# Performance work log

Hardware: AMD Instinct MI355X
Metric: run time of the kernel (lower is better)

The kernel has to match this reference:

```python
import jax, jax.numpy as jnp
import numpy as np

MARGIN = 0.3
WARMUP_EPOCHS = 10
K = 5
ALPHA = 2.0
SAME_CAM_NEG_BOOST = 1.2
NEG_INF = jnp.float32(-jnp.inf)
POS_INF = jnp.float32(jnp.inf)


def setup_inputs() -> dict:
    key = jax.random.key(0)
    k1, k2, k3 = jax.random.split(key, 3)
    N, D = 8192, 2048
    feats = jax.random.normal(k1, (N, D), dtype=jnp.float32)
    labels = jax.random.randint(k2, (N,), 0, 256, dtype=jnp.int64)
    camids = jax.random.randint(k3, (N,), 0, 8, dtype=jnp.int64)
    return {"feats": feats, "labels": labels, "camids": camids, "epoch": 20}


def _topk_mean(dist_mat, mask, k, largest):
    # dist_mat [N,N], mask [N,N] bool. Per-row mean of k largest/smallest valid elems.
    if largest:
        work = jnp.where(mask, dist_mat, NEG_INF)
        vals, _ = jax.lax.top_k(work, k)            # [N,k] largest
        fallback = jnp.max(work, axis=1)
    else:
        work = jnp.where(mask, dist_mat, POS_INF)
        vals = -jax.lax.top_k(-work, k)[0]          # [N,k] smallest
        fallback = jnp.min(work, axis=1)
    is_valid = jnp.isfinite(vals)
    safe_sum = jnp.sum(jnp.where(is_valid, vals, 0.0), axis=1)
    counts = jnp.maximum(is_valid.sum(axis=1), 1)
    mean = safe_sum / counts
    return jnp.where(is_valid.any(axis=1), mean, fallback)


def _forward(feats, labels, camids, epoch):
    # (1) L2 normalize
    norm = jnp.linalg.norm(feats, axis=-1, keepdims=True)
    x = feats / jnp.maximum(norm, 1e-12)
    # Euclidean distance matrix [N,N]
    sq = jnp.sum(x * x, axis=1)
    dist2 = sq[:, None] + sq[None, :] - 2.0 * (x @ x.T)
    dist = jnp.sqrt(jnp.maximum(dist2, 1e-12))
    # masks (constants w.r.t. grad)
    N = feats.shape[0]
    eye = jnp.eye(N, dtype=bool)
    same_label = labels[:, None] == labels[None, :]
    same_cam = camids[:, None] == camids[None, :]
    is_pos = same_label & ~eye & ~same_cam   # cross_cam_pos=True
    is_neg = ~same_label & ~eye
    # boosted same-camera negatives
    neg_bias = jnp.where(is_neg & same_cam, SAME_CAM_NEG_BOOST, 1.0)
    dist_neg_sel = dist / jnp.maximum(neg_bias, 1e-6)
    # (2) top-k hard mining
    d_ap = _topk_mean(dist, is_pos, K, largest=True)
    d_an = _topk_mean(dist_neg_sel, is_neg, K, largest=False)
    # (5) hardness-aware weighting (no grad)
    w = jax.lax.stop_gradient(jax.nn.sigmoid(ALPHA * (d_ap - d_an)))
    w = w / jnp.maximum(w.mean(), 1e-12)
    # (3) margin schedule
    if epoch is not None and epoch < WARMUP_EPOCHS:
        per_sample = jax.nn.softplus(-(d_an - d_ap))
    else:
        per_sample = jax.nn.relu(d_ap - d_an + MARGIN)  # MarginRankingLoss, y=1
    loss = jnp.mean(w * per_sample)
    return loss, jax.lax.stop_gradient(d_ap), jax.lax.stop_gradient(d_an)


def reference(feats, labels, camids, epoch):
    return _forward(feats, labels, camids, epoch)
```

## Files before the change

### kernel.cpp

```cpp
#include <hip/hip_runtime.h>
#include <hip/hip_bf16.h>
#include <stdint.h>

typedef float   floatx4  __attribute__((ext_vector_type(4)));
typedef float   floatx16 __attribute__((ext_vector_type(16)));
typedef int     intx4    __attribute__((ext_vector_type(4)));
typedef int     intx8    __attribute__((ext_vector_type(8)));
typedef _Float16 halfx8  __attribute__((ext_vector_type(8)));
typedef _Float16 halfx4  __attribute__((ext_vector_type(4)));
typedef _Float16 half2v  __attribute__((ext_vector_type(2)));

#define NROW 8192
#define NDIM 2048
#define BM 128
#define SLICE 64
#define NSLICE 32
#define NSTRIP 64
#define NTILE (NSTRIP*(NSTRIP+1)/2)
#define NPOSB 256
#define DT_LD 136
#define KL_SYM 64
#define SLOT_P 8
#define MERGE_BLOCKS 256
#define BOOST_INV 0.6944444444f

__device__ __forceinline__ void ins_desc(float (&a)[5], float v) {
#pragma unroll
    for (int k = 0; k < 5; ++k) { float hi = fmaxf(a[k], v); float lo = fminf(a[k], v); a[k] = hi; v = lo; }
}
__device__ __forceinline__ void ins_asc(float (&a)[5], float v) {
#pragma unroll
    for (int k = 0; k < 5; ++k) { float lo = fminf(a[k], v); float hi = fmaxf(a[k], v); a[k] = lo; v = hi; }
}

__device__ __forceinline__ int   h2bits(half2v v) { return __builtin_bit_cast(int, v); }
__device__ __forceinline__ half2v bits2h(int v)   { return __builtin_bit_cast(half2v, v); }
__device__ __forceinline__ void ins_desc2(half2v (&a)[5], half2v v) {
#pragma unroll
    for (int k = 0; k < 5; ++k) {
        half2v hi = __builtin_elementwise_max(a[k], v);
        half2v lo = __builtin_elementwise_min(a[k], v);
        a[k] = hi; v = lo;
    }
}
__device__ __forceinline__ void ins_asc2(half2v (&a)[5], half2v v) {
#pragma unroll
    for (int k = 0; k < 5; ++k) {
        half2v lo = __builtin_elementwise_min(a[k], v);
        half2v hi = __builtin_elementwise_max(a[k], v);
        a[k] = lo; v = hi;
    }
}

__device__ __forceinline__ void load_lds16(const void* g, void* l) {
    __builtin_amdgcn_global_load_lds((__attribute__((address_space(1))) void*)(void*)g,
                                     (__attribute__((address_space(3))) void*)l,
                                     16, 0, 0);
}

__global__ __launch_bounds__(256) void k_normalize(const float* __restrict__ feats,
                                                   unsigned char* __restrict__ xb,
                                                   float* __restrict__ sq) {
    const int lane = threadIdx.x & 63;
    const int row = (blockIdx.x << 2) + (threadIdx.x >> 6);
    const float* f = feats + (size_t)row * NDIM;
    float4 v[8];
    float ss = 0.f;
#pragma unroll
    for (int i = 0; i < 8; ++i) {
        v[i] = *(const float4*)(f + ((i << 6) + lane) * 4);
        ss += v[i].x * v[i].x + v[i].y * v[i].y + v[i].z * v[i].z + v[i].w * v[i].w;
    }
#pragma unroll
    for (int o = 32; o > 0; o >>= 1) ss += __shfl_xor(ss, o);
    float inv = 1.0f / fmaxf(sqrtf(ss), 1e-12f);
    if (lane == 0) sq[row] = ss * inv * inv;
    unsigned char* xo = xb + (size_t)row * NDIM;
#pragma unroll
    for (int i = 0; i < 8; ++i) {
        int w0 = __builtin_amdgcn_cvt_pk_fp8_f32(v[i].x * inv, v[i].y * inv, 0, false);
        w0     = __builtin_amdgcn_cvt_pk_fp8_f32(v[i].z * inv, v[i].w * inv, w0, true);
        *(int*)(xo + ((i << 6) + lane) * 4) = w0;
    }
}

__device__ __forceinline__ void scan_half_row_neg(const _Float16* Dt_,
        int srow, int shalf, float (&neg5)[5]) {
    const int s2 = 2 * (srow & 7);
    const int PINF2 = 0x7C007C00;
    half2v n5[5];
#pragma unroll
    for (int k = 0; k < 5; ++k) n5[k] = bits2h(PINF2);
#pragma unroll
    for (int c8 = 0; c8 < 8; ++c8) {
        const int pc = ((shalf * 8 + c8) + s2) & 15;
        intx4 v = *(const intx4*)(Dt_ + srow * DT_LD + pc * 8);
#pragma unroll
        for (int e = 0; e < 4; ++e) ins_asc2(n5, bits2h(v[e]));
    }
    half2v tn[5];
#pragma unroll
    for (int k = 0; k < 5; ++k)
        tn[k] = bits2h((int)__builtin_amdgcn_alignbit((unsigned)h2bits(n5[k]), (unsigned)h2bits(n5[k]), 16));
#pragma unroll
    for (int k = 0; k < 5; ++k) ins_asc2(n5, tn[k]);
#pragma unroll
    for (int k = 0; k < 5; ++k) neg5[k] = (float)n5[k][0];
}

__device__ __forceinline__ void emit_neg(float (&neg5)[5], int shalf,
        _Float16* negp, int gi, int slot) {
    float tn[5];
#pragma unroll
    for (int k = 0; k < 5; ++k) tn[k] = __shfl_xor(neg5[k], 1);
#pragma unroll
    for (int k = 0; k < 5; ++k) { if (tn[k] < neg5[4]) ins_asc(neg5, tn[k]); }
    if (shalf == 0) {
        const float PINF = __builtin_inff();
        halfx8 hn;
#pragma unroll
        for (int k = 0; k < 5; ++k) hn[k] = (_Float16)neg5[k];
        hn[5] = hn[6] = hn[7] = (_Float16)PINF;
        *(halfx8*)(negp + ((size_t)slot * NROW + gi) * SLOT_P) = hn;
    }
}

__global__ __launch_bounds__(256, 3) void k_main(
        const unsigned char* __restrict__ xb, const float* __restrict__ sq,
        const int* __restrict__ labels, const int* __restrict__ camids,
        _Float16* __restrict__ negp, _Float16* __restrict__ posf) {
    __shared__ __align__(16) char smem[51200];

    const int tid = threadIdx.x;
    const int w = tid >> 6, lane = tid & 63;
    const int m32 = lane & 31;
    const int hi = lane >> 5;
    const int key = (lane >> 1) & 3;
    const int p0 = ((2 * hi + key) & 3) * 16;
    const int p1 = ((2 * hi + 1 + key) & 3) * 16;
    const float FINF = __builtin_inff();
    const float NINF = -FINF;

    if (blockIdx.x < NPOSB) {
        char* stg0 = smem;
        _Float16* D2 = (_Float16*)(smem + 12288);
        int* mem = (int*)(smem + 21504);
        unsigned short* mlc = (unsigned short*)(smem + 21760);
        float* msq = (float*)(smem + 21888);
        int* cntp = (int*)(smem + 22144);

        const int L = blockIdx.x;
        if (tid == 0) *cntp = 0;
        __syncthreads();
        for (int i = tid; i < NROW; i += 256) {
            if (labels[i] == L) {
                int slot = atomicAdd(cntp, 1);
                if (slot < 64) mem[slot] = i;
            }
        }
        __syncthreads();
        const int cnt = min(*cntp, 64);
        if (tid < 64) {
            if (tid < cnt) {
                int gi = mem[tid];
                mlc[tid] = (unsigned short)((labels[gi] << 4) | camids[gi]);
                msq[tid] = sq[gi];
            } else {
                mem[tid] = 0; mlc[tid] = 0xFFFF; msq[tid] = 0.f;
            }
        }
        __syncthreads();

        const int wm = w >> 1, wn = w & 1;
        const int lr = lane >> 2;
        const int lcb = (((lane & 3) - ((lane >> 3) & 3)) & 3) * 16;
        const int myrow = mem[w * 16 + lr];

        auto pstage = [&](int buf, int koff) {
            load_lds16(xb + (size_t)myrow * NDIM + koff + lcb,
                       stg0 + (buf << 12) + w * 1024);
        };

        floatx16 acc;
#pragma unroll
        for (int r = 0; r < 16; ++r) acc[r] = 0.f;

        pstage(0, 0);
        pstage(1, SLICE);
        for (int s = 0; s < NSLICE; ++s) {
            if (s + 2 < NSLICE) {
                int bs = s + 2; bs -= (bs >= 3 ? 3 : 0); bs -= (bs >= 3 ? 3 : 0);
                pstage((s + 2) % 3, (s + 2) * SLICE);
            }
            if (s < NSLICE - 2)       asm volatile("s_waitcnt vmcnt(2)" ::: "memory");
            else if (s == NSLICE - 2) asm volatile("s_waitcnt vmcnt(1)" ::: "memory");
            else                      asm volatile("s_waitcnt vmcnt(0)" ::: "memory");
            __builtin_amdgcn_s_barrier();
            asm volatile("" ::: "memory");
            const char* Ab = stg0 + ((s % 3) << 12);
            const char* ap = Ab + (wm * 32 + m32) * SLICE;
            intx4 alo = *(const intx4*)(ap + p0);
            intx4 ahi = *(const intx4*)(ap + p1);
            intx8 af = __builtin_shufflevector(alo, ahi, 0, 1, 2, 3, 4, 5, 6, 7);
            const char* bp = Ab + (wn * 32 + m32) * SLICE;
            intx4 blo = *(const intx4*)(bp + p0);
            intx4 bhi = *(const intx4*)(bp + p1);
            intx8 bf = __builtin_shufflevector(blo, bhi, 0, 1, 2, 3, 4, 5, 6, 7);
            acc = __builtin_amdgcn_mfma_scale_f32_32x32x64_f8f6f4(af, bf, acc, 0, 0, 0, 127, 0, 127);
            asm volatile("" ::: "memory");
            __builtin_amdgcn_s_barrier();
            asm volatile("" ::: "memory");
        }

        {
            const int jl = (w & 1) * 32 + m32;
            const int lcj = (int)mlc[jl];
            const float sj = msq[jl];
            const int wm2 = w >> 1;
#pragma unroll
            for (int r = 0; r < 16; ++r) {
                const int il = wm2 * 32 + (r & 3) + 8 * (r >> 2) + 4 * hi;
                float d2 = fmaxf(msq[il] + sj - 2.0f * acc[r], 1e-12f);
                const int x = (int)mlc[il] ^ lcj;
                bool posv = ((x & 0xFFF0) == 0) & ((x & 15) != 0);
                D2[il * 72 + jl] = posv ? (_Float16)d2 : (_Float16)NINF;
            }
        }
        __syncthreads();

        {
            const int prow = tid >> 2, q = tid & 3;
            const int NINF2 = 0xFC00FC00;
            half2v p5h[5];
#pragma unroll
            for (int k = 0; k < 5; ++k) p5h[k] = bits2h(NINF2);
            const _Float16* dp = D2 + prow * 72 + q * 16;
            intx4 v0 = *(const intx4*)dp;
            intx4 v1 = *(const intx4*)(dp + 8);
#pragma unroll
            for (int e = 0; e < 4; ++e) ins_desc2(p5h, bits2h(v0[e]));
#pragma unroll
            for (int e = 0; e < 4; ++e) ins_desc2(p5h, bits2h(v1[e]));
            half2v tp[5];
#pragma unroll
            for (int k = 0; k < 5; ++k)
                tp[k] = bits2h((int)__builtin_amdgcn_alignbit((unsigned)h2bits(p5h[k]), (unsigned)h2bits(p5h[k]), 16));
#pragma unroll
            for (int k = 0; k < 5; ++k) ins_desc2(p5h, tp[k]);
            float p5[5];
#pragma unroll
            for (int k = 0; k < 5; ++k) p5[k] = (float)p5h[k][0];
#pragma unroll
            for (int o = 1; o <= 2; o <<= 1) {
                float tq[5];
#pragma unroll
                for (int k = 0; k < 5; ++k) tq[k] = __shfl_xor(p5[k], o);
#pragma unroll
                for (int k = 0; k < 5; ++k) { if (tq[k] > p5[4]) ins_desc(p5, tq[k]); }
            }
            if (q == 0 && prow < cnt) {
                halfx8 hp;
#pragma unroll
                for (int k = 0; k < 5; ++k) hp[k] = (_Float16)p5[k];
                hp[5] = hp[6] = hp[7] = (_Float16)NINF;
                *(halfx8*)(posf + (size_t)mem[prow] * SLOT_P) = hp;
            }
        }
        return;
    }

    _Float16* Dt = (_Float16*)smem;
    float* sqr_s = (float*)(smem + 49152);
    float* sqc_s = sqr_s + BM;
    unsigned short* labcam_a = (unsigned short*)(sqc_s + BM);
    unsigned short* labcam_b = labcam_a + BM;

    const int wm = w >> 1, wn = w & 1;

    int a, b;
    {
        int bx = blockIdx.x - NPOSB;
        int o = (bx & 7) * (NTILE / 8) + (bx >> 3);
        if (o < 1792) {
            int st = o >> 6;
            int SA = (int)((1.0f + sqrtf(8.0f * (float)st + 1.0f)) * 0.5f);
            while (SA * (SA - 1) / 2 > st) --SA;
            while (SA * (SA + 1) / 2 <= st) ++SA;
            int SB = st - SA * (SA - 1) / 2;
            int inner = o & 63;
            a = SA * 8 + (inner >> 3);
            b = SB * 8 + (inner & 7);
        } else {
            int idx = o - 1792;
            int st = idx / 36;
            int inner = idx - st * 36;
            int ia = (int)((sqrtf(8.0f * (float)inner + 1.0f) - 1.0f) * 0.5f);
            while (ia * (ia + 1) / 2 > inner) --ia;
            while ((ia + 1) * (ia + 2) / 2 <= inner) ++ia;
            int ib = inner - ia * (ia + 1) / 2;
            a = st * 8 + ia;
            b = st * 8 + ib;
        }
    }
    const int r0 = a * BM, c0 = b * BM;

    const int lr = lane >> 2;
    const int lc = (((lane & 3) - ((lane >> 3) & 3)) & 3) * 16;

    auto stage = [&](int buf, int koff) {
        char* Asb = smem + (buf << 14);
        char* Bsb = Asb + 8192;
#pragma unroll
        for (int q = 0; q < 2; ++q) {
            const int ra = w * 32 + q * 16;
            load_lds16(xb + (size_t)(r0 + ra + lr) * NDIM + koff + lc, Asb + ra * SLICE);
            load_lds16(xb + (size_t)(c0 + ra + lr) * NDIM + koff + lc, Bsb + ra * SLICE);
        }
    };

    if (tid < BM) {
        int gi = r0 + tid;
        sqr_s[tid] = sq[gi];
        labcam_a[tid] = (unsigned short)((labels[gi] << 4) | camids[gi]);
    } else {
        int t2 = tid - BM;
        int gj = c0 + t2;
        sqc_s[t2] = sq[gj];
        labcam_b[t2] = (unsigned short)((labels[gj] << 4) | camids[gj]);
    }

    stage(0, 0);
    stage(1, SLICE);

    const int srow = tid >> 1;
    const int shalf = tid & 1;

    floatx16 acc[2][2];
#pragma unroll
    for (int ti = 0; ti < 2; ++ti)
#pragma unroll
        for (int tj = 0; tj < 2; ++tj)
#pragma unroll
            for (int r = 0; r < 16; ++r) acc[ti][tj][r] = 0.f;

    int bc = 0;
    for (int s = 0; s < NSLICE; ++s) {
        if (s + 2 < NSLICE) {
            int bs = bc + 2; if (bs >= 3) bs -= 3;
            stage(bs, (s + 2) * SLICE);
        }
        if (s < NSLICE - 2)       asm volatile("s_waitcnt vmcnt(8)" ::: "memory");
        else if (s == NSLICE - 2) asm volatile("s_waitcnt vmcnt(4)" ::: "memory");
        else                      asm volatile("s_waitcnt vmcnt(0)" ::: "memory");
        __builtin_amdgcn_s_barrier();
        asm volatile("" ::: "memory");

        const char* Ab = smem + (bc << 14);
        const char* Bb = Ab + 8192;
        intx8 bf[2];
#pragma unroll
        for (int tj = 0; tj < 2; ++tj) {
            const char* bp = Bb + (wn * 64 + tj * 32 + m32) * SLICE;
            intx4 lo = *(const intx4*)(bp + p0);
            intx4 hi4 = *(const intx4*)(bp + p1);
            bf[tj] = __builtin_shufflevector(lo, hi4, 0, 1, 2, 3, 4, 5, 6, 7);
        }
        __builtin_amdgcn_s_setprio(1);
#pragma unroll
        for (int ti = 0; ti < 2; ++ti) {
            const char* ap = Ab + (wm * 64 + ti * 32 + m32) * SLICE;
            intx4 lo = *(const intx4*)(ap + p0);
            intx4 hi4 = *(const intx4*)(ap + p1);
            intx8 af = __builtin_shufflevector(lo, hi4, 0, 1, 2, 3, 4, 5, 6, 7);
            acc[ti][0] = __builtin_amdgcn_mfma_scale_f32_32x32x64_f8f6f4(
                af, bf[0], acc[ti][0], 0, 0, 0, 127, 0, 127);
            acc[ti][1] = __builtin_amdgcn_mfma_scale_f32_32x32x64_f8f6f4(
                af, bf[1], acc[ti][1], 0, 0, 0, 127, 0, 127);
        }
        __builtin_amdgcn_s_setprio(0);
        asm volatile("" ::: "memory");
        __builtin_amdgcn_s_barrier();
        asm volatile("" ::: "memory");
        bc = (bc + 1 == 3) ? 0 : bc + 1;
    }

    {
        const int jl0 = wn * 64 + m32, jl1 = jl0 + 32;
        const float sj0 = sqc_s[jl0], sj1 = sqc_s[jl1];
        const int lb0 = (int)labcam_b[jl0], lb1 = (int)labcam_b[jl1];
        const int jc0 = jl0 >> 3, j7_0 = jl0 & 7;
        const int jc1 = jl1 >> 3, j7_1 = jl1 & 7;
#pragma unroll
        for (int ti = 0; ti < 2; ++ti) {
#pragma unroll
            for (int r = 0; r < 16; ++r) {
                const int il = wm * 64 + ti * 32 + (r & 3) + 8 * (r >> 2) + 4 * hi;
                const float si = sqr_s[il];
                const int la = (int)labcam_a[il];
                const int rot = 2 * (il & 7);
                _Float16* drow = Dt + il * DT_LD;

                float d2 = fmaxf(si + sj0 - 2.0f * acc[ti][0][r], 1e-12f);
                int x = la ^ lb0;
                float nv = (x & 15) ? d2 : d2 * BOOST_INV;
                nv = (x & 0xFFF0) ? nv : FINF;
                acc[ti][0][r] = nv;
                drow[(((jc0 + rot) & 15) << 3) + j7_0] = (_Float16)nv;

                d2 = fmaxf(si + sj1 - 2.0f * acc[ti][1][r], 1e-12f);
                x = la ^ lb1;
                nv = (x & 15) ? d2 : d2 * BOOST_INV;
                nv = (x & 0xFFF0) ? nv : FINF;
                acc[ti][1][r] = nv;
                drow[(((jc1 + rot) & 15) << 3) + j7_1] = (_Float16)nv;
            }
        }
    }
    __syncthreads();

    float neg5[5];
    scan_half_row_neg(Dt, srow, shalf, neg5);
    emit_neg(neg5, shalf, negp, r0 + srow, b);

    if (a != b) {
        __syncthreads();
#pragma unroll
        for (int tj = 0; tj < 2; ++tj) {
#pragma unroll
            for (int ti = 0; ti < 2; ++ti) {
                const int jl = wn * 64 + tj * 32 + m32;
                const int cw2 = 2 * (jl & 7);
#pragma unroll
                for (int rq = 0; rq < 4; ++rq) {
                    const int base_row = wm * 64 + ti * 32 + 8 * rq + 4 * hi;
                    halfx4 h;
#pragma unroll
                    for (int e = 0; e < 4; ++e) h[e] = (_Float16)acc[ti][tj][rq * 4 + e];
                    const int pch = (((base_row >> 3) + cw2) & 15);
                    *(halfx4*)(Dt + jl * DT_LD + (pch << 3) + 4 * hi) = h;
                }
            }
        }
        __syncthreads();
        scan_half_row_neg(Dt, srow, shalf, neg5);
        emit_neg(neg5, shalf, negp, c0 + srow, a);
    }
}

__global__ __launch_bounds__(256) void k_merge_sym(const _Float16* __restrict__ negp,
        const _Float16* __restrict__ posf, const int* __restrict__ epoch_p,
        float* __restrict__ out, float* __restrict__ wsum_p, float* __restrict__ wpsum_p) {
    const int t = threadIdx.x;
    const int rl = t & 31;
    const int sg = t >> 5;
    const int row = blockIdx.x * 32 + rl;
    const float NINF = -__builtin_inff(), PINF = __builtin_inff();
    float n5[5] = {PINF, PINF, PINF, PINF, PINF};
    const size_t rbase = (size_t)row * SLOT_P;
#pragma unroll
    for (int s = 0; s < 8; ++s) {
        const size_t off = (size_t)(sg * 8 + s) * ((size_t)NROW * SLOT_P) + rbase;
        halfx8 nv = *(const halfx8*)(negp + off);
#pragma unroll
        for (int e = 0; e < 8; ++e) { float f = (float)nv[e]; if (f < n5[4]) ins_asc(n5, f); }
    }
    __shared__ __align__(16) _Float16 ln[32][8][8];
    const int sw = (sg + rl) & 7;
    {
        halfx8 hn;
#pragma unroll
        for (int k = 0; k < 5; ++k) hn[k] = (_Float16)n5[k];
        hn[5] = hn[6] = hn[7] = (_Float16)PINF;
        *(halfx8*)&ln[rl][sw][0] = hn;
    }
    __syncthreads();
    if (t < 32) {
        float N5[5] = {PINF, PINF, PINF, PINF, PINF};
#pragma unroll
        for (int g = 0; g < 8; ++g) {
            halfx8 nv = *(const halfx8*)&ln[t][g][0];
#pragma unroll
            for (int e = 0; e < 8; ++e) { float f = (float)nv[e]; if (f < N5[4]) ins_asc(N5, f); }
        }
        const int orow = blockIdx.x * 32 + t;
        halfx8 pv = *(const halfx8*)(posf + (size_t)orow * SLOT_P);
        float s = 0.f; int c = 0;
#pragma unroll
        for (int k = 0; k < 5; ++k) { float f = (float)pv[k]; bool fin = (f > NINF); s += fin ? sqrtf(f) : 0.f; c += fin ? 1 : 0; }
        float d_ap = (c > 0) ? s / (float)c : NINF;
        s = 0.f; c = 0;
#pragma unroll
        for (int k = 0; k < 5; ++k) { bool fin = (N5[k] < PINF); s += fin ? sqrtf(N5[k]) : 0.f; c += fin ? 1 : 0; }
        float d_an = (c > 0) ? s / (float)c : PINF;

        out[1 + orow] = d_ap;
        out[1 + NROW + orow] = d_an;
        float diff = d_ap - d_an;
        float w0 = 1.0f / (1.0f + expf(-2.0f * diff));
        float p;
        if (*epoch_p < 10) {
            p = fmaxf(diff, 0.0f) + log1pf(expf(-fabsf(diff)));
        } else {
            p = fmaxf(diff + 0.3f, 0.0f);
        }
        float wp = w0 * p;
#pragma unroll
        for (int o = 16; o > 0; o >>= 1) { w0 += __shfl_down(w0, o, 32); wp += __shfl_down(wp, o, 32); }
        if (t == 0) { wsum_p[blockIdx.x] = w0; wpsum_p[blockIdx.x] = wp; }
    }
}

__global__ void k_finalize(const float* __restrict__ wsum_p, const float* __restrict__ wpsum_p,
                           float* __restrict__ out) {
    const int t = threadIdx.x;
    float sw  = wsum_p[t] + wsum_p[t + 64] + wsum_p[t + 128] + wsum_p[t + 192];
    float swp = wpsum_p[t] + wpsum_p[t + 64] + wpsum_p[t + 128] + wpsum_p[t + 192];
#pragma unroll
    for (int o = 32; o > 0; o >>= 1) { sw += __shfl_down(sw, o); swp += __shfl_down(swp, o); }
    if (t == 0) {
        float M = fmaxf(sw / (float)NROW, 1e-12f);
        out[0] = swp / ((float)NROW * M);
    }
}

extern "C" void kernel_launch(void* const* d_in, const int* in_sizes, int n_in,
                              void* d_out, int out_size, void* d_ws, size_t ws_size,
                              hipStream_t stream) {
    const float* feats  = (const float*)d_in[0];
    const int*   labels = (const int*)d_in[1];
    const int*   camids = (const int*)d_in[2];
    const int*   epoch  = (const int*)d_in[3];
    float* out = (float*)d_out;
    char* ws = (char*)d_ws;

    unsigned char* xb = (unsigned char*)ws;
    float* sq = (float*)(ws + 16777216);
    const size_t NEG_HALVES = (size_t)KL_SYM * NROW * SLOT_P;
    _Float16* negp = (_Float16*)(ws + 16777216 + 32768);
    _Float16* posf = negp + NEG_HALVES;
    float* wsum_p  = (float*)((char*)(posf + (size_t)NROW * SLOT_P));
    float* wpsum_p = wsum_p + MERGE_BLOCKS;

    k_normalize<<<NROW / 4, 256, 0, stream>>>(feats, xb, sq);
    k_main<<<NPOSB + NTILE, 256, 0, stream>>>(xb, sq, labels, camids, negp, posf);
    k_merge_sym<<<MERGE_BLOCKS, 256, 0, stream>>>(negp, posf, epoch, out, wsum_p, wpsum_p);
    k_finalize<<<1, 64, 0, stream>>>(wsum_p, wpsum_p, out);
}
```

Baseline: 207.5 us.

## Load A operand directly into registers, stage only B through LDS

```diff
diff --git a/kernel.cpp b/kernel.cpp
--- a/kernel.cpp
+++ b/kernel.cpp
@@ -129,7 +129,7 @@
         const unsigned char* __restrict__ xb, const float* __restrict__ sq,
         const int* __restrict__ labels, const int* __restrict__ camids,
         _Float16* __restrict__ negp, _Float16* __restrict__ posf) {
-    __shared__ __align__(16) char smem[51200];
+    __shared__ __align__(16) char smem[36864];
 
     const int tid = threadIdx.x;
     const int w = tid >> 6, lane = tid & 63;
@@ -188,10 +188,7 @@
         pstage(0, 0);
         pstage(1, SLICE);
         for (int s = 0; s < NSLICE; ++s) {
-            if (s + 2 < NSLICE) {
-                int bs = s + 2; bs -= (bs >= 3 ? 3 : 0); bs -= (bs >= 3 ? 3 : 0);
-                pstage((s + 2) % 3, (s + 2) * SLICE);
-            }
+            if (s + 2 < NSLICE) pstage((s + 2) % 3, (s + 2) * SLICE);
             if (s < NSLICE - 2)       asm volatile("s_waitcnt vmcnt(2)" ::: "memory");
             else if (s == NSLICE - 2) asm volatile("s_waitcnt vmcnt(1)" ::: "memory");
             else                      asm volatile("s_waitcnt vmcnt(0)" ::: "memory");
@@ -270,7 +267,7 @@
     }
 
     _Float16* Dt = (_Float16*)smem;
-    float* sqr_s = (float*)(smem + 49152);
+    float* sqr_s = (float*)(smem + 34816);
     float* sqc_s = sqr_s + BM;
     unsigned short* labcam_a = (unsigned short*)(sqc_s + BM);
     unsigned short* labcam_b = labcam_a + BM;
@@ -304,20 +301,6 @@
     }
     const int r0 = a * BM, c0 = b * BM;
 
-    const int lr = lane >> 2;
-    const int lc = (((lane & 3) - ((lane >> 3) & 3)) & 3) * 16;
-
-    auto stage = [&](int buf, int koff) {
-        char* Asb = smem + (buf << 14);
-        char* Bsb = Asb + 8192;
-#pragma unroll
-        for (int q = 0; q < 2; ++q) {
-            const int ra = w * 32 + q * 16;
-            load_lds16(xb + (size_t)(r0 + ra + lr) * NDIM + koff + lc, Asb + ra * SLICE);
-            load_lds16(xb + (size_t)(c0 + ra + lr) * NDIM + koff + lc, Bsb + ra * SLICE);
-        }
-    };
-
     if (tid < BM) {
         int gi = r0 + tid;
         sqr_s[tid] = sq[gi];
@@ -329,8 +312,29 @@
         labcam_b[t2] = (unsigned short)((labels[gj] << 4) | camids[gj]);
     }
 
-    stage(0, 0);
-    stage(1, SLICE);
+    const int lr = lane >> 2;
+    const int lc = (((lane & 3) - ((lane >> 3) & 3)) & 3) * 16;
+    auto stageB = [&](int buf, int koff) {
+        char* Bsb = smem + (buf << 13);
+#pragma unroll
+        for (int q = 0; q < 2; ++q) {
+            const int ra = w * 32 + q * 16;
+            load_lds16(xb + (size_t)(c0 + ra + lr) * NDIM + koff + lc, Bsb + ra * SLICE);
+        }
+    };
+
+    const unsigned char* aptr0 = xb + (size_t)(r0 + wm * 64 + m32) * NDIM + hi * 32;
+    const unsigned char* aptr1 = aptr0 + (size_t)32 * NDIM;
+
+    intx4 xa0, xa1, xa2, xa3;
+    intx4 ya0, ya1, ya2, ya3;
+
+    stageB(0, 0);
+    xa0 = *(const intx4*)(aptr0);         xa1 = *(const intx4*)(aptr0 + 16);
+    xa2 = *(const intx4*)(aptr1);         xa3 = *(const intx4*)(aptr1 + 16);
+    stageB(1, SLICE);
+    ya0 = *(const intx4*)(aptr0 + SLICE); ya1 = *(const intx4*)(aptr0 + SLICE + 16);
+    ya2 = *(const intx4*)(aptr1 + SLICE); ya3 = *(const intx4*)(aptr1 + SLICE + 16);
 
     const int srow = tid >> 1;
     const int shalf = tid & 1;
@@ -343,46 +347,83 @@
 #pragma unroll
             for (int r = 0; r < 16; ++r) acc[ti][tj][r] = 0.f;
 
-    int bc = 0;
-    for (int s = 0; s < NSLICE; ++s) {
+    for (int s = 0; s < NSLICE; s += 2) {
         if (s + 2 < NSLICE) {
-            int bs = bc + 2; if (bs >= 3) bs -= 3;
-            stage(bs, (s + 2) * SLICE);
-        }
-        if (s < NSLICE - 2)       asm volatile("s_waitcnt vmcnt(8)" ::: "memory");
-        else if (s == NSLICE - 2) asm volatile("s_waitcnt vmcnt(4)" ::: "memory");
-        else                      asm volatile("s_waitcnt vmcnt(0)" ::: "memory");
+            stageB((s + 2) & 3, (s + 2) * SLICE);
+            asm volatile("s_waitcnt vmcnt(8)" ::: "memory");
+        } else {
+            asm volatile("s_waitcnt vmcnt(6)" ::: "memory");
+        }
         __builtin_amdgcn_s_barrier();
         asm volatile("" ::: "memory");
-
-        const char* Ab = smem + (bc << 14);
-        const char* Bb = Ab + 8192;
-        intx8 bf[2];
-#pragma unroll
-        for (int tj = 0; tj < 2; ++tj) {
-            const char* bp = Bb + (wn * 64 + tj * 32 + m32) * SLICE;
-            intx4 lo = *(const intx4*)(bp + p0);
-            intx4 hi4 = *(const intx4*)(bp + p1);
-            bf[tj] = __builtin_shufflevector(lo, hi4, 0, 1, 2, 3, 4, 5, 6, 7);
-        }
-        __builtin_amdgcn_s_setprio(1);
-#pragma unroll
-        for (int ti = 0; ti < 2; ++ti) {
-            const char* ap = Ab + (wm * 64 + ti * 32 + m32) * SLICE;
-            intx4 lo = *(const intx4*)(ap + p0);
-            intx4 hi4 = *(const intx4*)(ap + p1);
-            intx8 af = __builtin_shufflevector(lo, hi4, 0, 1, 2, 3, 4, 5, 6, 7);
-            acc[ti][0] = __builtin_amdgcn_mfma_scale_f32_32x32x64_f8f6f4(
-                af, bf[0], acc[ti][0], 0, 0, 0, 127, 0, 127);
-            acc[ti][1] = __builtin_amdgcn_mfma_scale_f32_32x32x64_f8f6f4(
-                af, bf[1], acc[ti][1], 0, 0, 0, 127, 0, 127);
-        }
-        __builtin_amdgcn_s_setprio(0);
-        asm volatile("" ::: "memory");
+        {
+            const char* Bb = smem + ((s & 3) << 13);
+            intx8 bf0, bf1;
+            {
+                const char* bp = Bb + (wn * 64 + m32) * SLICE;
+                intx4 lo = *(const intx4*)(bp + p0);
+                intx4 h4 = *(const intx4*)(bp + p1);
+                bf0 = __builtin_shufflevector(lo, h4, 0, 1, 2, 3, 4, 5, 6, 7);
+            }
+            {
+                const char* bp = Bb + (wn * 64 + 32 + m32) * SLICE;
+                intx4 lo = *(const intx4*)(bp + p0);
+                intx4 h4 = *(const intx4*)(bp + p1);
+                bf1 = __builtin_shufflevector(lo, h4, 0, 1, 2, 3, 4, 5, 6, 7);
+            }
+            __builtin_amdgcn_s_setprio(1);
+            intx8 af0 = __builtin_shufflevector(xa0, xa1, 0, 1, 2, 3, 4, 5, 6, 7);
+            intx8 af1 = __builtin_shufflevector(xa2, xa3, 0, 1, 2, 3, 4, 5, 6, 7);
+            acc[0][0] = __builtin_amdgcn_mfma_scale_f32_32x32x64_f8f6f4(af0, bf0, acc[0][0], 0, 0, 0, 127, 0, 127);
+            acc[0][1] = __builtin_amdgcn_mfma_scale_f32_32x32x64_f8f6f4(af0, bf1, acc[0][1], 0, 0, 0, 127, 0, 127);
+            acc[1][0] = __builtin_amdgcn_mfma_scale_f32_32x32x64_f8f6f4(af1, bf0, acc[1][0], 0, 0, 0, 127, 0, 127);
+            acc[1][1] = __builtin_amdgcn_mfma_scale_f32_32x32x64_f8f6f4(af1, bf1, acc[1][1], 0, 0, 0, 127, 0, 127);
+            __builtin_amdgcn_s_setprio(0);
+        }
+        if (s + 2 < NSLICE) {
+            const int ko = (s + 2) * SLICE;
+            xa0 = *(const intx4*)(aptr0 + ko); xa1 = *(const intx4*)(aptr0 + ko + 16);
+            xa2 = *(const intx4*)(aptr1 + ko); xa3 = *(const intx4*)(aptr1 + ko + 16);
+        }
+        if (s + 3 < NSLICE) {
+            stageB((s + 3) & 3, (s + 3) * SLICE);
+            asm volatile("s_waitcnt vmcnt(8)" ::: "memory");
+        } else {
+            asm volatile("s_waitcnt vmcnt(0)" ::: "memory");
+        }
         __builtin_amdgcn_s_barrier();
         asm volatile("" ::: "memory");
-        bc = (bc + 1 == 3) ? 0 : bc + 1;
-    }
+        {
+            const char* Bb = smem + (((s + 1) & 3) << 13);
+            intx8 bf0, bf1;
+            {
+                const char* bp = Bb + (wn * 64 + m32) * SLICE;
+                intx4 lo = *(const intx4*)(bp + p0);
+                intx4 h4 = *(const intx4*)(bp + p1);
+                bf0 = __builtin_shufflevector(lo, h4, 0, 1, 2, 3, 4, 5, 6, 7);
+            }
+            {
+                const char* bp = Bb + (wn * 64 + 32 + m32) * SLICE;
+                intx4 lo = *(const intx4*)(bp + p0);
+                intx4 h4 = *(const intx4*)(bp + p1);
+                bf1 = __builtin_shufflevector(lo, h4, 0, 1, 2, 3, 4, 5, 6, 7);
+            }
+            __builtin_amdgcn_s_setprio(1);
+            intx8 af0 = __builtin_shufflevector(ya0, ya1, 0, 1, 2, 3, 4, 5, 6, 7);
+            intx8 af1 = __builtin_shufflevector(ya2, ya3, 0, 1, 2, 3, 4, 5, 6, 7);
+            acc[0][0] = __builtin_amdgcn_mfma_scale_f32_32x32x64_f8f6f4(af0, bf0, acc[0][0], 0, 0, 0, 127, 0, 127);
+            acc[0][1] = __builtin_amdgcn_mfma_scale_f32_32x32x64_f8f6f4(af0, bf1, acc[0][1], 0, 0, 0, 127, 0, 127);
+            acc[1][0] = __builtin_amdgcn_mfma_scale_f32_32x32x64_f8f6f4(af1, bf0, acc[1][0], 0, 0, 0, 127, 0, 127);
+            acc[1][1] = __builtin_amdgcn_mfma_scale_f32_32x32x64_f8f6f4(af1, bf1, acc[1][1], 0, 0, 0, 127, 0, 127);
+            __builtin_amdgcn_s_setprio(0);
+        }
+        if (s + 3 < NSLICE) {
+            const int ko = (s + 3) * SLICE;
+            ya0 = *(const intx4*)(aptr0 + ko); ya1 = *(const intx4*)(aptr0 + ko + 16);
+            ya2 = *(const intx4*)(aptr1 + ko); ya3 = *(const intx4*)(aptr1 + ko + 16);
+        }
+    }
+    __syncthreads();
 
     {
         const int jl0 = wn * 64 + m32, jl1 = jl0 + 32;
```

After: 272.4 us. 31.3% more time.
